# Kernel tuning notes

Hardware: AMD Instinct MI355X
Metric: run time of the kernel (lower is better)

Reference implementation:

```python
import jax, jax.numpy as jnp
import numpy as np

N_NODES = 50000
N_EDGES = 800000
HID = 256
OUT = 128
NEG_SLOPE = 0.2


def gat_layer(x, src, dst, W_src, W_dst, a_src_vec, a_dst_vec, bias, n_nodes):
    # Dense projections (PyG lin_src / lin_dst for tuple in_channels)
    h_src = x @ W_src              # [N, C]
    h_dst = x @ W_dst              # [N, C]
    # Per-node attention logits (att_src/att_dst dot products)
    a_src = h_src @ a_src_vec      # [N]
    a_dst = h_dst @ a_dst_vec      # [N]
    # Edge logits + LeakyReLU
    e = jax.nn.leaky_relu(a_src[src] + a_dst[dst], NEG_SLOPE)  # [E]
    # Segment softmax over incoming edges of each dst node
    m = jax.ops.segment_max(e, dst, num_segments=n_nodes)      # [N]
    m = jnp.where(jnp.isfinite(m), m, 0.0)                      # empty segments
    ex = jnp.exp(e - m[dst])                                    # [E]
    s = jax.ops.segment_sum(ex, dst, num_segments=n_nodes)     # [N]
    alpha = ex / (s[dst] + 1e-16)                               # [E]
    # Attention-weighted message aggregation (scatter-add to dst)
    msg = alpha[:, None] * h_src[src]                           # [E, C]
    out = jax.ops.segment_sum(msg, dst, num_segments=n_nodes)  # [N, C]
    return out + bias


def setup_inputs() -> dict:
    key = jax.random.key(0)
    ks = jax.random.split(key, 12)
    x = jax.random.normal(ks[0], (N_NODES, HID), dtype=jnp.float32)
    edge_index = jax.random.randint(ks[1], (2, N_EDGES), 0, N_NODES, dtype=jnp.int64)
    sc1 = 1.0 / np.sqrt(HID)
    sc2 = 1.0 / np.sqrt(HID)
    return {
        "x": x,
        "edge_index": edge_index,
        "W1_src": jax.random.normal(ks[2], (HID, HID), dtype=jnp.float32) * sc1,
        "W1_dst": jax.random.normal(ks[3], (HID, HID), dtype=jnp.float32) * sc1,
        "att1_src": jax.random.normal(ks[4], (HID,), dtype=jnp.float32) * sc1,
        "att1_dst": jax.random.normal(ks[5], (HID,), dtype=jnp.float32) * sc1,
        "b1": jnp.zeros((HID,), dtype=jnp.float32),
        "W2_src": jax.random.normal(ks[6], (HID, OUT), dtype=jnp.float32) * sc2,
        "W2_dst": jax.random.normal(ks[7], (HID, OUT), dtype=jnp.float32) * sc2,
        "att2_src": jax.random.normal(ks[8], (OUT,), dtype=jnp.float32) * (1.0 / np.sqrt(OUT)),
        "att2_dst": jax.random.normal(ks[9], (OUT,), dtype=jnp.float32) * (1.0 / np.sqrt(OUT)),
        "b2": jnp.zeros((OUT,), dtype=jnp.float32),
    }


def reference(x, edge_index, W1_src, W1_dst, att1_src, att1_dst, b1,
              W2_src, W2_dst, att2_src, att2_dst, b2):
    src, dst = edge_index[0], edge_index[1]
    h = gat_layer(x, src, dst, W1_src, W1_dst, att1_src, att1_dst, b1, N_NODES)
    h = jax.nn.relu(h)
    out = gat_layer(h, src, dst, W2_src, W2_dst, att2_src, att2_dst, b2, N_NODES)
    return out
```

## Files before the change

kernel.cpp:

```cpp
#include <hip/hip_runtime.h>
#include <math.h>

#define N_NODES 50000
#define N_EDGES 800000
#define HID 256
#define OUT_C 128
#define NEG_SLOPE 0.2f
#define SCAN_NB ((N_NODES + 255) / 256)

typedef __attribute__((ext_vector_type(8))) short bf16x8;
typedef __attribute__((ext_vector_type(4))) float f32x4;
typedef _Float16 half_t;
typedef __attribute__((ext_vector_type(4))) _Float16 half4;
typedef __attribute__((ext_vector_type(2))) _Float16 half2t;

__device__ inline unsigned short bf16_rne(float x) {
    unsigned u = __float_as_uint(x);
    return (unsigned short)((u + 0x7fffu + ((u >> 16) & 1u)) >> 16);
}

__device__ __forceinline__ void async_copy16(const void* g, void* l) {
    __builtin_amdgcn_global_load_lds(
        (const __attribute__((address_space(1))) unsigned int*)g,
        (__attribute__((address_space(3))) unsigned int*)l, 16, 0, 0);
}


__global__ __launch_bounds__(256) void hist_rank_kernel(
    const int* __restrict__ dst, int* __restrict__ counts, int* __restrict__ rank) {
    int e = blockIdx.x * 256 + threadIdx.x;
    if (e < N_EDGES) rank[e] = atomicAdd(&counts[dst[e]], 1);
}

__global__ __launch_bounds__(256) void block_scan_kernel(
    const int* __restrict__ counts, int* __restrict__ excl,
    int* __restrict__ blockSums, int n) {
    __shared__ int waveSums[4];
    int i = blockIdx.x * 256 + threadIdx.x;
    int lane = threadIdx.x & 63;
    int wv = threadIdx.x >> 6;
    int c = (i < n) ? counts[i] : 0;
    int v = c;
    #pragma unroll
    for (int off = 1; off < 64; off <<= 1) {
        int t = __shfl_up(v, off);
        if (lane >= off) v += t;
    }
    if (lane == 63) waveSums[wv] = v;
    __syncthreads();
    int waveOff = 0;
    #pragma unroll
    for (int w = 0; w < 4; w++)
        if (w < wv) waveOff += waveSums[w];
    if (i < n) excl[i] = waveOff + v - c;
    if (threadIdx.x == 255) blockSums[blockIdx.x] = waveOff + v;
}

__global__ __launch_bounds__(256) void add_offsets_kernel(
    int* __restrict__ excl, const int* __restrict__ blockSums, int n) {
    __shared__ int lds[4];
    int tid = threadIdx.x;
    int partial = 0;
    for (int j = tid; j < (int)blockIdx.x; j += 256) partial += blockSums[j];
    #pragma unroll
    for (int off = 32; off > 0; off >>= 1) partial += __shfl_down(partial, off);
    if ((tid & 63) == 0) lds[tid >> 6] = partial;
    __syncthreads();
    int prefix = lds[0] + lds[1] + lds[2] + lds[3];
    int i = blockIdx.x * 256 + tid;
    if (i < n) excl[i] += prefix;
    if (i == 0) excl[n] = N_EDGES;
}

__global__ __launch_bounds__(256) void scatter_kernel(
    const int* __restrict__ src, const int* __restrict__ dst,
    const int* __restrict__ offsets, const int* __restrict__ rank,
    int* __restrict__ src_sorted) {
    int e = blockIdx.x * 256 + threadIdx.x;
    if (e >= N_EDGES) return;
    src_sorted[offsets[dst[e]] + rank[e]] = src[e];
}


__global__ __launch_bounds__(64) void compute_v_all_kernel(
    const float* __restrict__ W1s, const float* __restrict__ att1s,
    const float* __restrict__ W1d, const float* __restrict__ att1d,
    const float* __restrict__ W2s, const float* __restrict__ att2s,
    const float* __restrict__ W2d, const float* __restrict__ att2d,
    float* __restrict__ v1s, float* __restrict__ v1d,
    float* __restrict__ v2s, float* __restrict__ v2d) {
    int k = blockIdx.x;
    int lane = threadIdx.x;
    const float* W; const float* att; float* v; int cout;
    switch (blockIdx.y) {
        case 0: W = W1s; att = att1s; v = v1s; cout = HID; break;
        case 1: W = W1d; att = att1d; v = v1d; cout = HID; break;
        case 2: W = W2s; att = att2s; v = v2s; cout = OUT_C; break;
        default: W = W2d; att = att2d; v = v2d; cout = OUT_C; break;
    }
    float sum = 0.f;
    for (int j = lane; j < cout; j += 64)
        sum += W[k * cout + j] * att[j];
    #pragma unroll
    for (int off = 32; off > 0; off >>= 1)
        sum += __shfl_down(sum, off);
    if (lane == 0) v[k] = sum;
}


#define PACK1_T (8 * 17 * 64)
#define PACK2_T (8 * 9 * 64)

__global__ __launch_bounds__(256) void pack_all_kernel(
    const float* __restrict__ W1, const float* __restrict__ v1s, const float* __restrict__ v1d,
    const float* __restrict__ W2, const float* __restrict__ v2s, const float* __restrict__ v2d,
    unsigned short* __restrict__ hi1, unsigned short* __restrict__ lo1,
    unsigned short* __restrict__ hi2, unsigned short* __restrict__ lo2) {
    int t = blockIdx.x * 256 + threadIdx.x;
    const float *W, *vs, *vd; unsigned short *hi, *lo; int cout, NTL, tt;
    if (t < PACK1_T)            { tt = t;           W = W1; vs = v1s; vd = v1d; hi = hi1; lo = lo1; cout = HID;  NTL = 17; }
    else if (t < PACK1_T + PACK2_T) { tt = t - PACK1_T; W = W2; vs = v2s; vd = v2d; hi = hi2; lo = lo2; cout = OUT_C; NTL = 9; }
    else return;
    int lane = tt & 63;
    int tile = (tt >> 6) % NTL;
    int ks = tt / (64 * NTL);
    int m = lane & 15;
    int kbase = ks * 32 + (lane >> 4) * 8;
    #pragma unroll
    for (int j = 0; j < 8; j++) {
        float val;
        if (tile < NTL - 1) val = W[(kbase + j) * cout + tile * 16 + m];
        else val = (m == 0) ? vs[kbase + j] : (m == 1) ? vd[kbase + j] : 0.f;
        unsigned short h = bf16_rne(val);
        hi[tt * 8 + j] = h;
        lo[tt * 8 + j] = bf16_rne(val - __uint_as_float((unsigned)h << 16));
    }
}


template <int COUT, int NT, bool WRITE_A, bool ASPLIT>
__device__ __forceinline__ void gemm_body(
    const float* __restrict__ A,
    const unsigned short* __restrict__ Ahi, const unsigned short* __restrict__ Alo,
    const unsigned short* __restrict__ Bhi, const unsigned short* __restrict__ Blo,
    half_t* __restrict__ H,
    float* __restrict__ a_s, float* __restrict__ a_d, int M, int tile0,
    short* sBh, short* sBl) {
    const int NTL = COUT / 16 + 1;
    int wave = threadIdx.x >> 6, lane = threadIdx.x & 63;
    int m = lane & 15, quad = lane >> 4;
    int row0 = blockIdx.x * 128 + wave * 32;
    f32x4 acc[2][NT];
    #pragma unroll
    for (int rg = 0; rg < 2; rg++)
        #pragma unroll
        for (int nt = 0; nt < NT; nt++)
            acc[rg][nt] = (f32x4){0.f, 0.f, 0.f, 0.f};

    const float* arow[2];
    const unsigned short* arh[2];
    const unsigned short* arl[2];
    #pragma unroll
    for (int rg = 0; rg < 2; rg++) {
        int r = row0 + rg * 16 + m;
        if (r >= M) r = M - 1;
        if (ASPLIT) {
            arh[rg] = Ahi + (size_t)r * HID;
            arl[rg] = Alo + (size_t)r * HID;
        } else {
            arow[rg] = A + (size_t)r * HID;
        }
    }

    auto STAGE = [&](int ks, int b) {
        for (int u = wave; u < 2 * NT; u += 4) {
            int nt = (u < NT) ? u : u - NT;
            int tile = (WRITE_A && nt == NT - 1) ? (COUT / 16) : (tile0 + nt);
            size_t goff = ((size_t)(ks * NTL + tile) * 64 + lane) * 8;
            if (u < NT) async_copy16(Bhi + goff, sBh + b * NT * 512 + nt * 512);
            else        async_copy16(Blo + goff, sBl + b * NT * 512 + nt * 512);
        }
    };

    STAGE(0, 0);
    __syncthreads();
    int cur = 0;
    for (int ks = 0; ks < 8; ks++) {
        if (ks < 7) STAGE(ks + 1, cur ^ 1);

        bf16x8 ah[2], al[2];
        #pragma unroll
        for (int rg = 0; rg < 2; rg++) {
            if (ASPLIT) {
                ah[rg] = *(const bf16x8*)(arh[rg] + ks * 32 + quad * 8);
                al[rg] = *(const bf16x8*)(arl[rg] + ks * 32 + quad * 8);
            } else {
                const float* ap = arow[rg] + ks * 32 + quad * 8;
                float4 v0 = *(const float4*)ap;
                float4 v1 = *(const float4*)(ap + 4);
                float av[8] = {v0.x, v0.y, v0.z, v0.w, v1.x, v1.y, v1.z, v1.w};
                #pragma unroll
                for (int j = 0; j < 8; j++) {
                    unsigned short h = bf16_rne(av[j]);
                    float hf = __uint_as_float((unsigned)h << 16);
                    ah[rg][j] = (short)h;
                    al[rg][j] = (short)bf16_rne(av[j] - hf);
                }
            }
        }
        #pragma unroll
        for (int nt = 0; nt < NT; nt++) {
            bf16x8 bh = *(const bf16x8*)(sBh + cur * NT * 512 + nt * 512 + lane * 8);
            bf16x8 bl = *(const bf16x8*)(sBl + cur * NT * 512 + nt * 512 + lane * 8);
            acc[0][nt] = __builtin_amdgcn_mfma_f32_16x16x32_bf16(ah[0], bh, acc[0][nt], 0, 0, 0);
            acc[1][nt] = __builtin_amdgcn_mfma_f32_16x16x32_bf16(ah[1], bh, acc[1][nt], 0, 0, 0);
            acc[0][nt] = __builtin_amdgcn_mfma_f32_16x16x32_bf16(ah[0], bl, acc[0][nt], 0, 0, 0);
            acc[1][nt] = __builtin_amdgcn_mfma_f32_16x16x32_bf16(ah[1], bl, acc[1][nt], 0, 0, 0);
            acc[0][nt] = __builtin_amdgcn_mfma_f32_16x16x32_bf16(al[0], bh, acc[0][nt], 0, 0, 0);
            acc[1][nt] = __builtin_amdgcn_mfma_f32_16x16x32_bf16(al[1], bh, acc[1][nt], 0, 0, 0);
        }
        __syncthreads();
        cur ^= 1;
    }
    const int NW = WRITE_A ? NT - 1 : NT;
    #pragma unroll
    for (int rg = 0; rg < 2; rg++)
        #pragma unroll
        for (int nt = 0; nt < NW; nt++)
            #pragma unroll
            for (int r = 0; r < 4; r++) {
                int row = row0 + rg * 16 + quad * 4 + r;
                if (row < M)
                    H[(size_t)row * COUT + (tile0 + nt) * 16 + m] = (half_t)acc[rg][nt][r];
            }
    if (WRITE_A) {
        #pragma unroll
        for (int rg = 0; rg < 2; rg++)
            #pragma unroll
            for (int r = 0; r < 4; r++) {
                int row = row0 + rg * 16 + quad * 4 + r;
                if (row < M) {
                    if (m == 0) a_s[row] = acc[rg][NT - 1][r];
                    else if (m == 1) a_d[row] = acc[rg][NT - 1][r];
                }
            }
    }
}

template <int COUT, bool ASPLIT>
__global__ __launch_bounds__(256) void mfma_gemm_a_kernel(
    const float* __restrict__ A,
    const unsigned short* __restrict__ Ahi, const unsigned short* __restrict__ Alo,
    const unsigned short* __restrict__ Bhi, const unsigned short* __restrict__ Blo,
    half_t* __restrict__ H,
    float* __restrict__ a_s, float* __restrict__ a_d, int M) {
    __shared__ short sBh[2 * 9 * 512];
    __shared__ short sBl[2 * 9 * 512];
    if (blockIdx.y == 0)
        gemm_body<COUT, 9, true, ASPLIT>(A, Ahi, Alo, Bhi, Blo, H, a_s, a_d, M, 0, sBh, sBl);
    else
        gemm_body<COUT, 8, false, ASPLIT>(A, Ahi, Alo, Bhi, Blo, H, a_s, a_d, M, 8, sBh, sBl);
}


template <int C, bool RELU, bool OSPLIT>
__global__ __launch_bounds__(256) void fused_aggregate_kernel(
    const int* __restrict__ offsets, const int* __restrict__ src_sorted,
    const float* __restrict__ a_src, const float* __restrict__ a_dst,
    const half_t* __restrict__ h, const float* __restrict__ bias,
    float* __restrict__ out,
    unsigned short* __restrict__ outhi, unsigned short* __restrict__ outlo) {
    constexpr int CH = 8;
    int node = (int)((blockIdx.x * 256u + threadIdx.x) >> 6);
    int lane = threadIdx.x & 63;
    if (node >= N_NODES) return;
    int beg = offsets[node], end = offsets[node + 1];
    float ad = a_dst[node];
    float s = 0.f;

    if (C == 256) {
        float4 acc = make_float4(0.f, 0.f, 0.f, 0.f);
        for (int base = beg; base < end; base += CH) {
            int cnt = end - base; if (cnt > CH) cnt = CH;
            int idx[CH];
            #pragma unroll
            for (int j = 0; j < CH; j++)
                idx[j] = src_sorted[(j < cnt) ? base + j : base];
            half4 hv[CH];
            #pragma unroll
            for (int j = 0; j < CH; j++)
                hv[j] = *(const half4*)(h + ((unsigned)idx[j] * C + lane * 4));
            float w[CH];
            #pragma unroll
            for (int j = 0; j < CH; j++) {
                float l = a_src[idx[j]] + ad;
                l = fmaxf(l, l * NEG_SLOPE);
                w[j] = (j < cnt) ? __expf(l) : 0.f;
                s += w[j];
            }
            #pragma unroll
            for (int j = 0; j < CH; j++) {
                acc.x += w[j] * (float)hv[j][0]; acc.y += w[j] * (float)hv[j][1];
                acc.z += w[j] * (float)hv[j][2]; acc.w += w[j] * (float)hv[j][3];
            }
        }
        float inv = 1.f / (s + 1e-16f);
        float4 bv = *(const float4*)(bias + lane * 4);
        acc.x = acc.x * inv + bv.x; acc.y = acc.y * inv + bv.y;
        acc.z = acc.z * inv + bv.z; acc.w = acc.w * inv + bv.w;
        if (RELU) {
            acc.x = fmaxf(acc.x, 0.f); acc.y = fmaxf(acc.y, 0.f);
            acc.z = fmaxf(acc.z, 0.f); acc.w = fmaxf(acc.w, 0.f);
        }
        if (OSPLIT) {
            float o[4] = {acc.x, acc.y, acc.z, acc.w};
            ushort4 h4, l4;
            unsigned short* hp = (unsigned short*)&h4;
            unsigned short* lp = (unsigned short*)&l4;
            #pragma unroll
            for (int j = 0; j < 4; j++) {
                unsigned short hh = bf16_rne(o[j]);
                hp[j] = hh;
                lp[j] = bf16_rne(o[j] - __uint_as_float((unsigned)hh << 16));
            }
            *(ushort4*)(outhi + (size_t)node * C + lane * 4) = h4;
            *(ushort4*)(outlo + (size_t)node * C + lane * 4) = l4;
        } else {
            *(float4*)(out + (size_t)node * C + lane * 4) = acc;
        }
    } else {
        float2 acc = make_float2(0.f, 0.f);
        for (int base = beg; base < end; base += CH) {
            int cnt = end - base; if (cnt > CH) cnt = CH;
            int idx[CH];
            #pragma unroll
            for (int j = 0; j < CH; j++)
                idx[j] = src_sorted[(j < cnt) ? base + j : base];
            half2t hv[CH];
            #pragma unroll
            for (int j = 0; j < CH; j++)
                hv[j] = *(const half2t*)(h + ((unsigned)idx[j] * C + lane * 2));
            float w[CH];
            #pragma unroll
            for (int j = 0; j < CH; j++) {
                float l = a_src[idx[j]] + ad;
                l = fmaxf(l, l * NEG_SLOPE);
                w[j] = (j < cnt) ? __expf(l) : 0.f;
                s += w[j];
            }
            #pragma unroll
            for (int j = 0; j < CH; j++) {
                acc.x += w[j] * (float)hv[j][0]; acc.y += w[j] * (float)hv[j][1];
            }
        }
        float inv = 1.f / (s + 1e-16f);
        float2 bv = *(const float2*)(bias + lane * 2);
        acc.x = acc.x * inv + bv.x; acc.y = acc.y * inv + bv.y;
        if (RELU) { acc.x = fmaxf(acc.x, 0.f); acc.y = fmaxf(acc.y, 0.f); }
        *(float2*)(out + (size_t)node * C + lane * 2) = acc;
    }
}

extern "C" void kernel_launch(void* const* d_in, const int* in_sizes, int n_in,
                              void* d_out, int out_size, void* d_ws, size_t ws_size,
                              hipStream_t stream) {
    const float* x     = (const float*)d_in[0];
    const int*   edge  = (const int*)d_in[1];
    const int*   src   = edge;
    const int*   dst   = edge + N_EDGES;
    const float* W1s   = (const float*)d_in[2];
    const float* W1d   = (const float*)d_in[3];
    const float* att1s = (const float*)d_in[4];
    const float* att1d = (const float*)d_in[5];
    const float* b1    = (const float*)d_in[6];
    const float* W2s   = (const float*)d_in[7];
    const float* W2d   = (const float*)d_in[8];
    const float* att2s = (const float*)d_in[9];
    const float* att2d = (const float*)d_in[10];
    const float* b2    = (const float*)d_in[11];
    float* out = (float*)d_out;

    float* ws    = (float*)d_ws;
    half_t* h1   = (half_t*)ws;
    unsigned short* act2hi = (unsigned short*)(ws + (size_t)N_NODES * HID);
    unsigned short* act2lo = act2hi + (size_t)N_NODES * HID;
    float* a_s   = ws + 2 * (size_t)N_NODES * HID;
    float* a_d   = a_s + N_NODES;
    float* vbuf  = a_d + N_NODES;
    int* ibase      = (int*)(vbuf + 4 * HID);
    int* src_sorted = ibase;
    int* rank       = src_sorted + N_EDGES;
    int* counts     = rank + N_EDGES;
    int* offsets    = counts + N_NODES;
    int* blockSums  = offsets + N_NODES + 1;
    unsigned short* wp1h = (unsigned short*)(((uintptr_t)(blockSums + SCAN_NB) + 15) & ~(uintptr_t)15);
    unsigned short* wp1l = wp1h + PACK1_T * 8;
    unsigned short* wp2h = wp1l + PACK1_T * 8;
    unsigned short* wp2l = wp2h + PACK2_T * 8;
    float* v1s = vbuf, *v1d = vbuf + HID, *v2s = vbuf + 2 * HID, *v2d = vbuf + 3 * HID;
    half_t* h2 = h1;

    const int edgeBlocks = (N_EDGES + 255) / 256;
    const int waveBlocksN = (N_NODES + 3) / 4;
    const int gemmBlocks = (N_NODES + 127) / 128;

    hipMemsetAsync(counts, 0, N_NODES * sizeof(int), stream);
    hist_rank_kernel<<<edgeBlocks, 256, 0, stream>>>(dst, counts, rank);
    block_scan_kernel<<<SCAN_NB, 256, 0, stream>>>(counts, offsets, blockSums, N_NODES);
    add_offsets_kernel<<<SCAN_NB, 256, 0, stream>>>(offsets, blockSums, N_NODES);
    scatter_kernel<<<edgeBlocks, 256, 0, stream>>>(src, dst, offsets, rank, src_sorted);

    compute_v_all_kernel<<<dim3(HID, 4), 64, 0, stream>>>(
        W1s, att1s, W1d, att1d, W2s, att2s, W2d, att2d, v1s, v1d, v2s, v2d);
    pack_all_kernel<<<(PACK1_T + PACK2_T + 255) / 256, 256, 0, stream>>>(
        W1s, v1s, v1d, W2s, v2s, v2d, wp1h, wp1l, wp2h, wp2l);

    mfma_gemm_a_kernel<HID, false><<<dim3(gemmBlocks, 2), 256, 0, stream>>>(
        x, nullptr, nullptr, wp1h, wp1l, h1, a_s, a_d, N_NODES);
    fused_aggregate_kernel<HID, true, true><<<waveBlocksN, 256, 0, stream>>>(
        offsets, src_sorted, a_s, a_d, h1, b1, nullptr, act2hi, act2lo);

    mfma_gemm_a_kernel<OUT_C, true><<<dim3(gemmBlocks, 1), 256, 0, stream>>>(
        nullptr, act2hi, act2lo, wp2h, wp2l, h2, a_s, a_d, N_NODES);
    fused_aggregate_kernel<OUT_C, false, false><<<waveBlocksN, 256, 0, stream>>>(
        offsets, src_sorted, a_s, a_d, h2, b2, out, nullptr, nullptr);
}
```

Baseline: 319.5 us.

## Merge scatter, attention-vector and weight-pack kernels; use smaller row tiles for layer-2 GEMM

Folds the edge scatter, the W·att vector reduction and the bf16 hi/lo weight packing into one prep_kernel launch. The attention-vector blocks now write their packed tile directly, so the intermediate v buffer and one dependency step go away. The GEMM row-group count becomes a template parameter, and layer 2 uses 64-row blocks so it launches twice as many blocks for the narrower output. This removes two launches and serial gaps, and raises occupancy on the small GEMM, at the cost of reloading B tiles more often per row.

```diff
diff --git a/kernel.cpp b/kernel.cpp
--- a/kernel.cpp
+++ b/kernel.cpp
@@ -72,73 +72,82 @@
     if (i == 0) excl[n] = N_EDGES;
 }
 
-__global__ __launch_bounds__(256) void scatter_kernel(
+
+#define PACK1_T (8 * 17 * 64)
+#define PACK2_T (8 * 9 * 64)
+#define EDGE_BLOCKS ((N_EDGES + 255) / 256)
+#define PACK_BLOCKS ((PACK1_T + PACK2_T + 255) / 256)
+#define V_BLOCKS 128
+
+__global__ __launch_bounds__(256) void prep_kernel(
     const int* __restrict__ src, const int* __restrict__ dst,
     const int* __restrict__ offsets, const int* __restrict__ rank,
-    int* __restrict__ src_sorted) {
-    int e = blockIdx.x * 256 + threadIdx.x;
-    if (e >= N_EDGES) return;
-    src_sorted[offsets[dst[e]] + rank[e]] = src[e];
-}
-
-
-__global__ __launch_bounds__(64) void compute_v_all_kernel(
+    int* __restrict__ src_sorted,
     const float* __restrict__ W1s, const float* __restrict__ att1s,
     const float* __restrict__ W1d, const float* __restrict__ att1d,
     const float* __restrict__ W2s, const float* __restrict__ att2s,
     const float* __restrict__ W2d, const float* __restrict__ att2d,
-    float* __restrict__ v1s, float* __restrict__ v1d,
-    float* __restrict__ v2s, float* __restrict__ v2d) {
-    int k = blockIdx.x;
-    int lane = threadIdx.x;
-    const float* W; const float* att; float* v; int cout;
-    switch (blockIdx.y) {
-        case 0: W = W1s; att = att1s; v = v1s; cout = HID; break;
-        case 1: W = W1d; att = att1d; v = v1d; cout = HID; break;
-        case 2: W = W2s; att = att2s; v = v2s; cout = OUT_C; break;
-        default: W = W2d; att = att2d; v = v2d; cout = OUT_C; break;
-    }
-    float sum = 0.f;
-    for (int j = lane; j < cout; j += 64)
-        sum += W[k * cout + j] * att[j];
-    #pragma unroll
-    for (int off = 32; off > 0; off >>= 1)
-        sum += __shfl_down(sum, off);
-    if (lane == 0) v[k] = sum;
-}
-
-
-#define PACK1_T (8 * 17 * 64)
-#define PACK2_T (8 * 9 * 64)
-
-__global__ __launch_bounds__(256) void pack_all_kernel(
-    const float* __restrict__ W1, const float* __restrict__ v1s, const float* __restrict__ v1d,
-    const float* __restrict__ W2, const float* __restrict__ v2s, const float* __restrict__ v2d,
     unsigned short* __restrict__ hi1, unsigned short* __restrict__ lo1,
     unsigned short* __restrict__ hi2, unsigned short* __restrict__ lo2) {
-    int t = blockIdx.x * 256 + threadIdx.x;
-    const float *W, *vs, *vd; unsigned short *hi, *lo; int cout, NTL, tt;
-    if (t < PACK1_T)            { tt = t;           W = W1; vs = v1s; vd = v1d; hi = hi1; lo = lo1; cout = HID;  NTL = 17; }
-    else if (t < PACK1_T + PACK2_T) { tt = t - PACK1_T; W = W2; vs = v2s; vd = v2d; hi = hi2; lo = lo2; cout = OUT_C; NTL = 9; }
-    else return;
-    int lane = tt & 63;
-    int tile = (tt >> 6) % NTL;
-    int ks = tt / (64 * NTL);
-    int m = lane & 15;
-    int kbase = ks * 32 + (lane >> 4) * 8;
-    #pragma unroll
-    for (int j = 0; j < 8; j++) {
-        float val;
-        if (tile < NTL - 1) val = W[(kbase + j) * cout + tile * 16 + m];
-        else val = (m == 0) ? vs[kbase + j] : (m == 1) ? vd[kbase + j] : 0.f;
+    if (blockIdx.x < EDGE_BLOCKS) {
+        int e = blockIdx.x * 256 + threadIdx.x;
+        if (e < N_EDGES)
+            src_sorted[offsets[dst[e]] + rank[e]] = src[e];
+        return;
+    }
+    if (blockIdx.x < EDGE_BLOCKS + PACK_BLOCKS) {
+        int t = (blockIdx.x - EDGE_BLOCKS) * 256 + threadIdx.x;
+        const float *W; unsigned short *hi, *lo; int cout, NTL, tt;
+        if (t < PACK1_T)            { tt = t;           W = W1s; hi = hi1; lo = lo1; cout = HID;  NTL = 17; }
+        else if (t < PACK1_T + PACK2_T) { tt = t - PACK1_T; W = W2s; hi = hi2; lo = lo2; cout = OUT_C; NTL = 9; }
+        else return;
+        int lane = tt & 63;
+        int tile = (tt >> 6) % NTL;
+        if (tile == NTL - 1) return;
+        int ks = tt / (64 * NTL);
+        int m = lane & 15;
+        int kbase = ks * 32 + (lane >> 4) * 8;
+        #pragma unroll
+        for (int j = 0; j < 8; j++) {
+            float val = W[(size_t)(kbase + j) * cout + tile * 16 + m];
+            unsigned short h = bf16_rne(val);
+            hi[tt * 8 + j] = h;
+            lo[tt * 8 + j] = bf16_rne(val - __uint_as_float((unsigned)h << 16));
+        }
+        return;
+    }
+    int vb = blockIdx.x - EDGE_BLOCKS - PACK_BLOCKS;
+    int layer = vb >> 6;
+    int wave = threadIdx.x >> 6, lane = threadIdx.x & 63;
+    int k = (vb & 63) * 4 + wave;
+    const float *Ws, *Wd, *as_, *ad_; unsigned short *hi, *lo; int cout, NTL;
+    if (layer == 0) { Ws = W1s; Wd = W1d; as_ = att1s; ad_ = att1d; hi = hi1; lo = lo1; cout = HID;  NTL = 17; }
+    else            { Ws = W2s; Wd = W2d; as_ = att2s; ad_ = att2d; hi = hi2; lo = lo2; cout = OUT_C; NTL = 9; }
+    float vs = 0.f, vd = 0.f;
+    for (int j = lane; j < cout; j += 64) {
+        vs += Ws[(size_t)k * cout + j] * as_[j];
+        vd += Wd[(size_t)k * cout + j] * ad_[j];
+    }
+    #pragma unroll
+    for (int off = 32; off > 0; off >>= 1) {
+        vs += __shfl_down(vs, off);
+        vd += __shfl_down(vd, off);
+    }
+    vs = __shfl(vs, 0);
+    vd = __shfl(vd, 0);
+    int ks = k >> 5, quad = (k >> 3) & 3, j = k & 7;
+    if (lane < 32) {
+        int m = lane & 15;
+        int tt = ks * 64 * NTL + (NTL - 1) * 64 + quad * 16 + m;
+        float val = (m == 0) ? vs : (m == 1) ? vd : 0.f;
         unsigned short h = bf16_rne(val);
-        hi[tt * 8 + j] = h;
-        lo[tt * 8 + j] = bf16_rne(val - __uint_as_float((unsigned)h << 16));
-    }
-}
-
-
-template <int COUT, int NT, bool WRITE_A, bool ASPLIT>
+        if (lane < 16) hi[tt * 8 + j] = h;
+        else           lo[tt * 8 + j] = bf16_rne(val - __uint_as_float((unsigned)h << 16));
+    }
+}
+
+
+template <int COUT, int NT, int RG, bool WRITE_A, bool ASPLIT>
 __device__ __forceinline__ void gemm_body(
     const float* __restrict__ A,
     const unsigned short* __restrict__ Ahi, const unsigned short* __restrict__ Alo,
@@ -149,19 +158,19 @@
     const int NTL = COUT / 16 + 1;
     int wave = threadIdx.x >> 6, lane = threadIdx.x & 63;
     int m = lane & 15, quad = lane >> 4;
-    int row0 = blockIdx.x * 128 + wave * 32;
-    f32x4 acc[2][NT];
-    #pragma unroll
-    for (int rg = 0; rg < 2; rg++)
+    int row0 = blockIdx.x * (RG * 64) + wave * (RG * 16);
+    f32x4 acc[RG][NT];
+    #pragma unroll
+    for (int rg = 0; rg < RG; rg++)
         #pragma unroll
         for (int nt = 0; nt < NT; nt++)
             acc[rg][nt] = (f32x4){0.f, 0.f, 0.f, 0.f};
 
-    const float* arow[2];
-    const unsigned short* arh[2];
-    const unsigned short* arl[2];
-    #pragma unroll
-    for (int rg = 0; rg < 2; rg++) {
+    const float* arow[RG];
+    const unsigned short* arh[RG];
+    const unsigned short* arl[RG];
+    #pragma unroll
+    for (int rg = 0; rg < RG; rg++) {
         int r = row0 + rg * 16 + m;
         if (r >= M) r = M - 1;
         if (ASPLIT) {
@@ -188,9 +197,9 @@
     for (int ks = 0; ks < 8; ks++) {
         if (ks < 7) STAGE(ks + 1, cur ^ 1);
 
-        bf16x8 ah[2], al[2];
-        #pragma unroll
-        for (int rg = 0; rg < 2; rg++) {
+        bf16x8 ah[RG], al[RG];
+        #pragma unroll
+        for (int rg = 0; rg < RG; rg++) {
             if (ASPLIT) {
                 ah[rg] = *(const bf16x8*)(arh[rg] + ks * 32 + quad * 8);
                 al[rg] = *(const bf16x8*)(arl[rg] + ks * 32 + quad * 8);
@@ -212,19 +221,19 @@
         for (int nt = 0; nt < NT; nt++) {
             bf16x8 bh = *(const bf16x8*)(sBh + cur * NT * 512 + nt * 512 + lane * 8);
             bf16x8 bl = *(const bf16x8*)(sBl + cur * NT * 512 + nt * 512 + lane * 8);
-            acc[0][nt] = __builtin_amdgcn_mfma_f32_16x16x32_bf16(ah[0], bh, acc[0][nt], 0, 0, 0);
-            acc[1][nt] = __builtin_amdgcn_mfma_f32_16x16x32_bf16(ah[1], bh, acc[1][nt], 0, 0, 0);
-            acc[0][nt] = __builtin_amdgcn_mfma_f32_16x16x32_bf16(ah[0], bl, acc[0][nt], 0, 0, 0);
-            acc[1][nt] = __builtin_amdgcn_mfma_f32_16x16x32_bf16(ah[1], bl, acc[1][nt], 0, 0, 0);
-            acc[0][nt] = __builtin_amdgcn_mfma_f32_16x16x32_bf16(al[0], bh, acc[0][nt], 0, 0, 0);
-            acc[1][nt] = __builtin_amdgcn_mfma_f32_16x16x32_bf16(al[1], bh, acc[1][nt], 0, 0, 0);
+            #pragma unroll
+            for (int rg = 0; rg < RG; rg++) {
+                acc[rg][nt] = __builtin_amdgcn_mfma_f32_16x16x32_bf16(ah[rg], bh, acc[rg][nt], 0, 0, 0);
+                acc[rg][nt] = __builtin_amdgcn_mfma_f32_16x16x32_bf16(ah[rg], bl, acc[rg][nt], 0, 0, 0);
+                acc[rg][nt] = __builtin_amdgcn_mfma_f32_16x16x32_bf16(al[rg], bh, acc[rg][nt], 0, 0, 0);
+            }
         }
         __syncthreads();
         cur ^= 1;
     }
     const int NW = WRITE_A ? NT - 1 : NT;
     #pragma unroll
-    for (int rg = 0; rg < 2; rg++)
+    for (int rg = 0; rg < RG; rg++)
         #pragma unroll
         for (int nt = 0; nt < NW; nt++)
             #pragma unroll
@@ -235,7 +244,7 @@
             }
     if (WRITE_A) {
         #pragma unroll
-        for (int rg = 0; rg < 2; rg++)
+        for (int rg = 0; rg < RG; rg++)
             #pragma unroll
             for (int r = 0; r < 4; r++) {
                 int row = row0 + rg * 16 + quad * 4 + r;
@@ -247,7 +256,7 @@
     }
 }
 
-template <int COUT, bool ASPLIT>
+template <int COUT, int RG, bool ASPLIT>
 __global__ __launch_bounds__(256) void mfma_gemm_a_kernel(
     const float* __restrict__ A,
     const unsigned short* __restrict__ Ahi, const unsigned short* __restrict__ Alo,
@@ -257,9 +266,9 @@
     __shared__ short sBh[2 * 9 * 512];
     __shared__ short sBl[2 * 9 * 512];
     if (blockIdx.y == 0)
-        gemm_body<COUT, 9, true, ASPLIT>(A, Ahi, Alo, Bhi, Blo, H, a_s, a_d, M, 0, sBh, sBl);
+        gemm_body<COUT, 9, RG, true, ASPLIT>(A, Ahi, Alo, Bhi, Blo, H, a_s, a_d, M, 0, sBh, sBl);
     else
-        gemm_body<COUT, 8, false, ASPLIT>(A, Ahi, Alo, Bhi, Blo, H, a_s, a_d, M, 8, sBh, sBl);
+        gemm_body<COUT, 8, RG, false, ASPLIT>(A, Ahi, Alo, Bhi, Blo, H, a_s, a_d, M, 8, sBh, sBl);
 }
 
 
@@ -386,8 +395,7 @@
     unsigned short* act2lo = act2hi + (size_t)N_NODES * HID;
     float* a_s   = ws + 2 * (size_t)N_NODES * HID;
     float* a_d   = a_s + N_NODES;
-    float* vbuf  = a_d + N_NODES;
-    int* ibase      = (int*)(vbuf + 4 * HID);
+    int* ibase      = (int*)(a_d + N_NODES);
     int* src_sorted = ibase;
     int* rank       = src_sorted + N_EDGES;
     int* counts     = rank + N_EDGES;
@@ -397,30 +405,28 @@
     unsigned short* wp1l = wp1h + PACK1_T * 8;
     unsigned short* wp2h = wp1l + PACK1_T * 8;
     unsigned short* wp2l = wp2h + PACK2_T * 8;
-    float* v1s = vbuf, *v1d = vbuf + HID, *v2s = vbuf + 2 * HID, *v2d = vbuf + 3 * HID;
     half_t* h2 = h1;
 
-    const int edgeBlocks = (N_EDGES + 255) / 256;
     const int waveBlocksN = (N_NODES + 3) / 4;
-    const int gemmBlocks = (N_NODES + 127) / 128;
+    const int gemmBlocks1 = (N_NODES + 127) / 128;
+    const int gemmBlocks2 = (N_NODES + 63) / 64;
 
     hipMemsetAsync(counts, 0, N_NODES * sizeof(int), stream);
-    hist_rank_kernel<<<edgeBlocks, 256, 0, stream>>>(dst, counts, rank);
+    hist_rank_kernel<<<EDGE_BLOCKS, 256, 0, stream>>>(dst, counts, rank);
     block_scan_kernel<<<SCAN_NB, 256, 0, stream>>>(counts, offsets, blockSums, N_NODES);
     add_offsets_kernel<<<SCAN_NB, 256, 0, stream>>>(offsets, blockSums, N_NODES);
-    scatter_kernel<<<edgeBlocks, 256, 0, stream>>>(src, dst, offsets, rank, src_sorted);
-
-    compute_v_all_kernel<<<dim3(HID, 4), 64, 0, stream>>>(
-        W1s, att1s, W1d, att1d, W2s, att2s, W2d, att2d, v1s, v1d, v2s, v2d);
-    pack_all_kernel<<<(PACK1_T + PACK2_T + 255) / 256, 256, 0, stream>>>(
-        W1s, v1s, v1d, W2s, v2s, v2d, wp1h, wp1l, wp2h, wp2l);
-
-    mfma_gemm_a_kernel<HID, false><<<dim3(gemmBlocks, 2), 256, 0, stream>>>(
+
+    prep_kernel<<<EDGE_BLOCKS + PACK_BLOCKS + V_BLOCKS, 256, 0, stream>>>(
+        src, dst, offsets, rank, src_sorted,
+        W1s, att1s, W1d, att1d, W2s, att2s, W2d, att2d,
+        wp1h, wp1l, wp2h, wp2l);
+
+    mfma_gemm_a_kernel<HID, 2, false><<<dim3(gemmBlocks1, 2), 256, 0, stream>>>(
         x, nullptr, nullptr, wp1h, wp1l, h1, a_s, a_d, N_NODES);
     fused_aggregate_kernel<HID, true, true><<<waveBlocksN, 256, 0, stream>>>(
         offsets, src_sorted, a_s, a_d, h1, b1, nullptr, act2hi, act2lo);
 
-    mfma_gemm_a_kernel<OUT_C, true><<<dim3(gemmBlocks, 1), 256, 0, stream>>>(
+    mfma_gemm_a_kernel<OUT_C, 1, true><<<dim3(gemmBlocks2, 1), 256, 0, stream>>>(
         nullptr, act2hi, act2lo, wp2h, wp2l, h2, a_s, a_d, N_NODES);
     fused_aggregate_kernel<OUT_C, false, false><<<waveBlocksN, 256, 0, stream>>>(
         offsets, src_sorted, a_s, a_d, h2, b2, out, nullptr, nullptr);
```

Measured after the change: 304.9 us. 4.6% less time.
